# Optimization experiments

Measured on AMD Instinct MI355X. Metric: run time of the kernel, lower is better.

Reference implementation:

```python
import jax, jax.numpy as jnp
import numpy as np

N, FIN, H, C, D = 50000, 128, 4, 64, 4
E = 800000


def leaky_relu(x, slope):
    return jnp.where(x >= 0, x, slope * x)


def gat_layer(x, src, dst, W, A, att_src, att_dst, bias):
    # x: [N, Fin]; W: [Fin, H*C]; A: [Fin, H*D]; att_*: [H, D]; bias: [C]
    n = x.shape[0]
    h = (x @ W).reshape(n, H, -1)          # [N, H, C] message features
    a = (x @ A).reshape(n, H, -1)          # [N, H, D] attention features
    alpha_src = jnp.einsum('nhd,hd->nh', a, att_src)   # [N, H]
    alpha_dst = jnp.einsum('nhd,hd->nh', a, att_dst)   # [N, H]
    e = leaky_relu(alpha_src[src] + alpha_dst[dst], 0.2)  # [E, H]
    # edge softmax over incoming edges of each destination node
    m = jax.ops.segment_max(e, dst, num_segments=n)       # [N, H]
    ex = jnp.exp(e - m[dst])                               # [E, H]
    denom = jax.ops.segment_sum(ex, dst, num_segments=n)  # [N, H]
    w = ex / denom[dst]                                    # [E, H]
    msg = h[src] * w[..., None]                            # [E, H, C]
    out = jax.ops.segment_sum(msg, dst, num_segments=n)   # [N, H, C]
    return out.mean(axis=1) + bias                         # head-average -> [N, C]


def setup_inputs() -> dict:
    key = jax.random.key(0)
    ks = jax.random.split(key, 12)
    x = jax.random.normal(ks[0], (N, FIN), dtype=jnp.float32)
    edge_index = jax.random.randint(ks[1], (2, E), 0, N, dtype=jnp.int64)
    s = 0.05
    return {
        'x': x,
        'edge_index': edge_index,
        'W1': jax.random.normal(ks[2], (FIN, H * C), dtype=jnp.float32) * s,
        'A1': jax.random.normal(ks[3], (FIN, H * D), dtype=jnp.float32) * s,
        'att_src1': jax.random.normal(ks[4], (H, D), dtype=jnp.float32) * s,
        'att_dst1': jax.random.normal(ks[5], (H, D), dtype=jnp.float32) * s,
        'b1': jnp.zeros((C,), dtype=jnp.float32),
        'W2': jax.random.normal(ks[6], (C, H * C), dtype=jnp.float32) * s,
        'A2': jax.random.normal(ks[7], (C, H * D), dtype=jnp.float32) * s,
        'att_src2': jax.random.normal(ks[8], (H, D), dtype=jnp.float32) * s,
        'att_dst2': jax.random.normal(ks[9], (H, D), dtype=jnp.float32) * s,
        'b2': jnp.zeros((C,), dtype=jnp.float32),
    }


def reference(x, edge_index, W1, A1, att_src1, att_dst1, b1, W2, A2, att_src2, att_dst2, b2):
    src, dst = edge_index[0], edge_index[1]
    x = gat_layer(x, src, dst, W1, A1, att_src1, att_dst1, b1)
    x = leaky_relu(x, 0.1)
    x = gat_layer(x, src, dst, W2, A2, att_src2, att_dst2, b2)
    x = leaky_relu(x, 0.1)
    return x
```

## Files before the change

### kernel.cpp

```cpp
#include <hip/hip_runtime.h>


#define N_NODES 50000
#define N_EDGES 800000
#define CAP 64
#define NB_SC4 782
#define NB_NODE1 782
#define NB_SETUP 197

typedef __attribute__((ext_vector_type(8))) short short8;
typedef __attribute__((ext_vector_type(8))) _Float16 f16x8;
typedef __attribute__((ext_vector_type(4))) float f32x4;
typedef __attribute__((ext_vector_type(8))) unsigned short ushort8;
typedef __attribute__((ext_vector_type(4))) unsigned short us4v;

__device__ __forceinline__ float bf2f(unsigned short u){
  return __uint_as_float(((unsigned int)u) << 16);
}
__device__ __forceinline__ unsigned short f2bf(float f){
  unsigned int u = __float_as_uint(f);
  u = (u + 0x7FFFu + ((u >> 16) & 1u)) >> 16;
  return (unsigned short)u;
}
__device__ __forceinline__ float ldf(const void* p, int i, bool bf){
  return bf ? bf2f(((const unsigned short*)p)[i]) : ((const float*)p)[i];
}

struct SetupPtrs {
  const void *W1, *A1, *aS1, *aD1, *b1, *W2, *A2, *aS2, *aD2, *b2, *x;
};


__device__ __forceinline__ void nodeA1_body(int nblk, int tid,
    const void* __restrict__ xin_, const void* __restrict__ A1,
    const void* __restrict__ aS1, const void* __restrict__ aD1,
    float* __restrict__ alpha_s, float* __restrict__ alpha_d)
{
  const int F = 128, STR = F + 8, KT = 4, CH = F / 8;
  __shared__ unsigned short xs[64 * 136];
  __shared__ unsigned short BsdL[2048];
  __shared__ int sbf;
  const int base = nblk * 64;
  if (tid < 64){
    unsigned int wv = ((const unsigned int*)xin_)[tid] & 0xFFFFu;
    unsigned int ex = (wv >> 7) & 0xFFu;
    bool hit = (ex >= 100u && ex <= 135u);
    unsigned long long mm = __ballot(hit);
    if (tid == 0) sbf = (__popcll(mm) > 40) ? 1 : 0;
  }
  __syncthreads();
  const bool bf = (sbf != 0);

  {
    const int lane = tid & 63, kt = tid >> 6, c = lane & 15;
    ushort8 v8;
    #pragma unroll
    for (int j = 0; j < 8; ++j){
      int k = kt * 32 + (lane >> 4) * 8 + j;
      float v = 0.f;
      if (c < 4){
        #pragma unroll
        for (int dd = 0; dd < 4; ++dd)
          v += ldf(A1, k * 16 + c * 4 + dd, bf) * ldf(aS1, c * 4 + dd, bf);
      } else if (c < 8){
        int hh = c - 4;
        #pragma unroll
        for (int dd = 0; dd < 4; ++dd)
          v += ldf(A1, k * 16 + hh * 4 + dd, bf) * ldf(aD1, hh * 4 + dd, bf);
      }
      v8[j] = f2bf(v);
    }
    *(ushort8*)&BsdL[tid * 8] = v8;
  }

  for (int v = tid; v < 64 * CH; v += 256){
    int row = v / CH, c8 = v % CH;
    int node = base + row; if (node >= N_NODES) node = N_NODES - 1;
    size_t g = (size_t)node * F + c8 * 8;
    ushort8 u;
    if (bf){
      u = *(const ushort8*)((const unsigned short*)xin_ + g);
    } else {
      const float* xf = (const float*)xin_ + g;
      float4 f0 = *(const float4*)xf, f1 = *(const float4*)(xf + 4);
      u[0]=f2bf(f0.x); u[1]=f2bf(f0.y); u[2]=f2bf(f0.z); u[3]=f2bf(f0.w);
      u[4]=f2bf(f1.x); u[5]=f2bf(f1.y); u[6]=f2bf(f1.z); u[7]=f2bf(f1.w);
    }
    *(ushort8*)&xs[row * STR + c8 * 8] = u;
  }
  __syncthreads();

  const int wave = tid >> 6, l = tid & 63;
  const int quad = l >> 4, m = l & 15;
  const int wbase = base + wave * 16;

  f32x4 aacc = (f32x4)0.f;
  #pragma unroll
  for (int kt = 0; kt < KT; ++kt){
    short8 af = *(const short8*)&xs[(wave * 16 + m) * STR + kt * 32 + quad * 8];
    short8 sd = *(const short8*)&BsdL[((size_t)kt * 64 + l) * 8];
    aacc = __builtin_amdgcn_mfma_f32_16x16x32_bf16(af, sd, aacc, 0, 0, 0);
  }
  if (m < 8){
    float* dstp = (m < 4) ? alpha_s : alpha_d;
    int hh = m & 3;
    #pragma unroll
    for (int r = 0; r < 4; ++r){
      int node = wbase + quad * 4 + r;
      if (node < N_NODES) dstp[node * 4 + hh] = aacc[r];
    }
  }
}


__global__ __launch_bounds__(256) void k_mega(SetupPtrs S,
    const int* __restrict__ src, const int* __restrict__ dst,
    int* __restrict__ fill, unsigned short* __restrict__ csr,
    float* __restrict__ alpha_s, float* __restrict__ alpha_d,
    _Float16* __restrict__ Wb1f, _Float16* __restrict__ Wb2f,
    unsigned short* __restrict__ Bsd2f,
    float* __restrict__ bc1, float* __restrict__ bc2,
    int* __restrict__ flag)
{
  const int b = blockIdx.x, tid = threadIdx.x;
  if (b < NB_SC4){
    const int ebase = b * 1024 + tid;
    int d[4], s[4];
    #pragma unroll
    for (int i = 0; i < 4; ++i){
      int e = ebase + i * 256;
      bool ok = (e < N_EDGES);
      d[i] = ok ? dst[e] : -1;
      s[i] = ok ? src[e] : 0;
    }
    #pragma unroll
    for (int i = 0; i < 4; ++i){
      if (d[i] >= 0){
        int r = atomicAdd(&fill[d[i]], 1);
        if (r < CAP) csr[((unsigned)d[i] << 6) + r] = (unsigned short)s[i];
      }
    }
    return;
  }
  if (b < NB_SC4 + NB_NODE1){
    nodeA1_body(b - NB_SC4, tid, S.x, S.A1, S.aS1, S.aD1, alpha_s, alpha_d);
    return;
  }
  __shared__ int sbf;
  if (tid < 64){
    unsigned int w = ((const unsigned int*)S.x)[tid] & 0xFFFFu;
    unsigned int e = (w >> 7) & 0xFFu;
    bool hit = (e >= 100u && e <= 135u);
    unsigned long long m = __ballot(hit);
    if (tid == 0) sbf = (__popcll(m) > 40) ? 1 : 0;
  }
  __syncthreads();
  const bool bf = (sbf != 0);
  const int bw = b - NB_SC4 - NB_NODE1;
  if (bw < 128){
    int t = bw * 256 + tid;
    int j = t & 7, lane = (t >> 3) & 63, kt = (t >> 9) & 15, nt = t >> 13;
    int q = kt * 32 + (lane >> 4) * 8 + j;
    int c = nt * 16 + (lane & 15);
    int h = q >> 7, f = q & 127;
    Wb1f[t] = (_Float16)(0.25f * ldf(S.W1, f * 256 + h * 64 + c, bf));
  } else if (bw < 192){
    int t = (bw - 128) * 256 + tid;
    int j = t & 7, lane = (t >> 3) & 63, kt = (t >> 9) & 7, nt = t >> 12;
    int q = kt * 32 + (lane >> 4) * 8 + j;
    int c = nt * 16 + (lane & 15);
    int h = q >> 6, f = q & 63;
    Wb2f[t] = (_Float16)(0.25f * ldf(S.W2, f * 256 + h * 64 + c, bf));
  } else if (bw < 196){
    int t = (bw - 192) * 256 + tid;
    int j = t & 7, lane = (t >> 3) & 63, kt = t >> 9;
    int k = kt * 32 + (lane >> 4) * 8 + j;
    int c = lane & 15;
    float v = 0.f;
    if (c < 4){
      for (int dd = 0; dd < 4; ++dd)
        v += ldf(S.A2, k * 16 + c * 4 + dd, bf) * ldf(S.aS2, c * 4 + dd, bf);
    } else if (c < 8){
      int h = c - 4;
      for (int dd = 0; dd < 4; ++dd)
        v += ldf(S.A2, k * 16 + h * 4 + dd, bf) * ldf(S.aD2, h * 4 + dd, bf);
    }
    Bsd2f[t] = f2bf(v);
  } else {
    if (tid < 64)       bc1[tid] = ldf(S.b1, tid, bf);
    else if (tid < 128) bc2[tid - 64] = ldf(S.b2, tid - 64, bf);
    else if (tid == 128) *flag = bf ? 1 : 0;
  }
}


template<int FIN, bool BF>
__device__ __forceinline__ void ldrow(const void* xg, unsigned s, int f0,
                                      float (&out)[FIN / 16])
{
  const int NFL = FIN / 16;
  if (BF){
    const unsigned short* p = (const unsigned short*)xg + (size_t)s * FIN + f0;
    if (NFL == 8){
      ushort8 u = *(const ushort8*)p;
      #pragma unroll
      for (int j = 0; j < NFL; ++j) out[j] = bf2f(u[j]);
    } else {
      us4v u = *(const us4v*)p;
      #pragma unroll
      for (int j = 0; j < NFL; ++j) out[j] = bf2f(u[j]);
    }
  } else {
    const float* p = (const float*)xg + (size_t)s * FIN + f0;
    #pragma unroll
    for (int j = 0; j < NFL; ++j) out[j] = p[j];
  }
}

template<int FIN, bool BF, int STR>
__device__ __forceinline__ void aggr_phase1(const void* __restrict__ xg,
    const float* __restrict__ alpha_s, const float* __restrict__ alpha_d,
    const int* __restrict__ fill, const unsigned short* __restrict__ csr,
    _Float16* __restrict__ ylds, int base, int w, int l)
{
  const int NFL = FIN / 16;
  const int h = l >> 4, sub = l & 15, f0 = sub * NFL;
  #pragma unroll 1
  for (int r = 0; r < 4; ++r){
    const int n = base + w * 4 + r;
    const float adv = alpha_d[n * 4 + h];
    float den = 0.f;
    float acc[NFL];
    #pragma unroll
    for (int j = 0; j < NFL; ++j) acc[j] = 0.f;

    int cnt = fill[n]; if (cnt > CAP) cnt = CAP;
    const unsigned short* cp = csr + ((unsigned)n << 6);
    int p = 0;
    for (; p + 8 <= cnt; p += 8){
      ushort8 s8 = *(const ushort8*)(cp + p);
      float a[8];
      float v[8][NFL];
      #pragma unroll
      for (int i = 0; i < 8; ++i){
        unsigned s = s8[i];
        a[i] = alpha_s[s * 4 + h];
        ldrow<FIN, BF>(xg, s, f0, v[i]);
      }
      #pragma unroll
      for (int i = 0; i < 8; ++i){
        float e = a[i] + adv; e = fmaxf(e, 0.2f * e); float wt = __expf(e);
        den += wt;
        #pragma unroll
        for (int j = 0; j < NFL; ++j) acc[j] += wt * v[i][j];
      }
    }
    if (p + 4 <= cnt){
      ushort4 s4 = *(const ushort4*)(cp + p);
      unsigned sx = s4.x, sy = s4.y, sz = s4.z, sw = s4.w;
      float ax = alpha_s[sx * 4 + h];
      float ay = alpha_s[sy * 4 + h];
      float az = alpha_s[sz * 4 + h];
      float aw = alpha_s[sw * 4 + h];
      float vx[NFL], vy[NFL], vz[NFL], vw[NFL];
      ldrow<FIN, BF>(xg, sx, f0, vx);
      ldrow<FIN, BF>(xg, sy, f0, vy);
      ldrow<FIN, BF>(xg, sz, f0, vz);
      ldrow<FIN, BF>(xg, sw, f0, vw);
      float e0 = ax + adv; e0 = fmaxf(e0, 0.2f * e0); float w0 = __expf(e0);
      float e1 = ay + adv; e1 = fmaxf(e1, 0.2f * e1); float w1 = __expf(e1);
      float e2 = az + adv; e2 = fmaxf(e2, 0.2f * e2); float w2 = __expf(e2);
      float e3 = aw + adv; e3 = fmaxf(e3, 0.2f * e3); float w3 = __expf(e3);
      den += w0; den += w1; den += w2; den += w3;
      #pragma unroll
      for (int j = 0; j < NFL; ++j)
        acc[j] += w0 * vx[j] + w1 * vy[j] + w2 * vz[j] + w3 * vw[j];
      p += 4;
    }
    for (; p < cnt; ++p){
      unsigned s = cp[p];
      float a = alpha_s[s * 4 + h];
      float v0[NFL];
      ldrow<FIN, BF>(xg, s, f0, v0);
      float e = a + adv; e = fmaxf(e, 0.2f * e); float wgt = __expf(e);
      den += wgt;
      #pragma unroll
      for (int j = 0; j < NFL; ++j) acc[j] += wgt * v0[j];
    }
    const float rh = (den > 0.f) ? (1.f / den) : 0.f;
    const int row = w * 4 + r;
    _Float16* yp = &ylds[row * STR + h * FIN + f0];
    #pragma unroll
    for (int j = 0; j < NFL; ++j) yp[j] = (_Float16)(acc[j] * rh);
  }
}

template<int FIN, int MODE>
__global__ __launch_bounds__(256) void k_aggrX(
    const void* __restrict__ xg,
    const float* __restrict__ alpha_s, const float* __restrict__ alpha_d,
    const int* __restrict__ fill, const unsigned short* __restrict__ csr,
    const _Float16* __restrict__ Wf,
    const float* __restrict__ bias, void* __restrict__ out,
    const int* __restrict__ flag,
    const unsigned short* __restrict__ Bsd2f,
    float* __restrict__ as2, float* __restrict__ ad2)
{
  const int K = 4 * FIN, KT = K / 32, STR = K + 8;
  __shared__ _Float16 ylds[16 * (4 * FIN + 8)];
  __shared__ unsigned short x2t[16 * 72];
  const int tid = threadIdx.x, w = tid >> 6, l = tid & 63;
  const int base = blockIdx.x * 16;

  if (MODE == 0 && *flag == 0)
    aggr_phase1<FIN, false, STR>(xg, alpha_s, alpha_d, fill, csr, ylds, base, w, l);
  else
    aggr_phase1<FIN, true,  STR>(xg, alpha_s, alpha_d, fill, csr, ylds, base, w, l);
  __syncthreads();

  const int quad = l >> 4, m = l & 15;
  const int nt = w;
  f32x4 cacc = (f32x4)0.f;
  #pragma unroll
  for (int kt = 0; kt < KT; ++kt){
    f16x8 av = *(const f16x8*)&ylds[m * STR + kt * 32 + quad * 8];
    f16x8 bv = *(const f16x8*)(Wf + ((size_t)(nt * KT + kt) * 64 + l) * 8);
    cacc = __builtin_amdgcn_mfma_f32_16x16x32_f16(av, bv, cacc, 0, 0, 0);
  }
  const int c = nt * 16 + m;
  const float bs = bias[c];
  #pragma unroll
  for (int r2 = 0; r2 < 4; ++r2){
    int node = base + quad * 4 + r2;
    float v = cacc[r2] + bs;
    v = fmaxf(v, 0.1f * v);
    if (MODE == 0){
      unsigned short o = f2bf(v);
      ((unsigned short*)out)[(size_t)node * 64 + c] = o;
      x2t[(quad * 4 + r2) * 72 + c] = o;
    } else {
      if (*flag) ((unsigned short*)out)[(size_t)node * 64 + c] = f2bf(v);
      else       ((float*)out)[(size_t)node * 64 + c] = v;
    }
  }

  if (MODE == 0){
    __syncthreads();
    if (w == 0){
      f32x4 aacc = (f32x4)0.f;
      #pragma unroll
      for (int kt = 0; kt < 2; ++kt){
        short8 af = *(const short8*)&x2t[m * 72 + kt * 32 + quad * 8];
        short8 sd = *(const short8*)(Bsd2f + ((size_t)kt * 64 + l) * 8);
        aacc = __builtin_amdgcn_mfma_f32_16x16x32_bf16(af, sd, aacc, 0, 0, 0);
      }
      if (m < 8){
        float* dstp = (m < 4) ? as2 : ad2;
        int hh = m & 3;
        #pragma unroll
        for (int r = 0; r < 4; ++r){
          int node = base + quad * 4 + r;
          dstp[node * 4 + hh] = aacc[r];
        }
      }
    }
  }
}


extern "C" void kernel_launch(void* const* d_in, const int* in_sizes, int n_in,
                              void* d_out, int out_size, void* d_ws, size_t ws_size,
                              hipStream_t stream)
{
  const void* x  = d_in[0];
  const int* ei  = (const int*)d_in[1];
  const int* src = ei;
  const int* dst = ei + N_EDGES;

  char* ws = (char*)d_ws;
  unsigned short* csr = (unsigned short*)(ws);
  unsigned short* x2  = (unsigned short*)(ws + 6400000);
  float* as_    = (float*)(ws + 12800000);
  float* ad_    = (float*)(ws + 13600000);
  float* as2_   = (float*)(ws + 14400000);
  float* ad2_   = (float*)(ws + 15200000);
  int*   fill   = (int*)  (ws + 16000000);
  _Float16* Wb1f = (_Float16*)(ws + 16200000);
  _Float16* Wb2f = (_Float16*)(ws + 16265536);
  unsigned short* Bsd2f = (unsigned short*)(ws + 16298304);
  float* bc1    = (float*)(ws + 16300352);
  float* bc2    = (float*)(ws + 16300608);
  int*   flag   = (int*)  (ws + 16300864);

  hipMemsetAsync(fill, 0, N_NODES * sizeof(int), stream);

  SetupPtrs S;
  S.W1 = d_in[2];  S.A1 = d_in[3];  S.aS1 = d_in[4];  S.aD1 = d_in[5];  S.b1 = d_in[6];
  S.W2 = d_in[7];  S.A2 = d_in[8];  S.aS2 = d_in[9];  S.aD2 = d_in[10]; S.b2 = d_in[11];
  S.x  = x;

  k_mega<<<NB_SC4 + NB_NODE1 + NB_SETUP, 256, 0, stream>>>(
      S, src, dst, fill, csr, as_, ad_, Wb1f, Wb2f, Bsd2f, bc1, bc2, flag);

  k_aggrX<128, 0><<<N_NODES / 16, 256, 0, stream>>>(
      x, as_, ad_, fill, csr, Wb1f, bc1, x2, flag, Bsd2f, as2_, ad2_);

  k_aggrX<64, 1><<<N_NODES / 16, 256, 0, stream>>>(
      x2, as2_, ad2_, fill, csr, Wb2f, bc2, d_out, flag, Bsd2f, as2_, ad2_);
}
```

Before: 298.9 us.

## Bucket incoming edges by source-index slice and gather in sorted slice order

The CSR build now splits each destination's edge list into 8 buckets keyed by the high bits of the source index. The aggregation kernel compacts these buckets into shared memory, then walks the slices in order across all four rows of a wave, so gathers of source rows land in a narrower address range at a time, which should improve cache locality. The costs are an 8x larger fill counter array with a bigger memset, extra shared-memory staging with two barriers, and a 16-edge cap per slice that could drop edges for nodes whose incoming edges cluster in one slice.

```diff
diff --git a/kernel.cpp b/kernel.cpp
--- a/kernel.cpp
+++ b/kernel.cpp
@@ -3,7 +3,9 @@
 
 #define N_NODES 50000
 #define N_EDGES 800000
-#define CAP 64
+#define SLICES 8
+#define SCAP 16
+#define NCAP 64
 #define NB_SC4 782
 #define NB_NODE1 782
 #define NB_SETUP 197
@@ -136,8 +138,10 @@
     #pragma unroll
     for (int i = 0; i < 4; ++i){
       if (d[i] >= 0){
-        int r = atomicAdd(&fill[d[i]], 1);
-        if (r < CAP) csr[((unsigned)d[i] << 6) + r] = (unsigned short)s[i];
+        unsigned sl = ((unsigned)s[i]) >> 13;
+        unsigned bidx = (unsigned)d[i] * SLICES + sl;
+        int r = atomicAdd(&fill[bidx], 1);
+        if (r < SCAP) csr[(bidx << 4) + r] = (unsigned short)s[i];
       }
     }
     return;
@@ -220,78 +224,67 @@
 template<int FIN, bool BF, int STR>
 __device__ __forceinline__ void aggr_phase1(const void* __restrict__ xg,
     const float* __restrict__ alpha_s, const float* __restrict__ alpha_d,
-    const int* __restrict__ fill, const unsigned short* __restrict__ csr,
+    const unsigned short (*__restrict__ els)[NCAP], const int (*__restrict__ sst)[SLICES + 1],
     _Float16* __restrict__ ylds, int base, int w, int l)
 {
   const int NFL = FIN / 16;
   const int h = l >> 4, sub = l & 15, f0 = sub * NFL;
-  #pragma unroll 1
+  const int j0 = w * 4;
+
+  float den[4] = {0.f, 0.f, 0.f, 0.f};
+  float acc[4][NFL];
+  #pragma unroll
+  for (int r = 0; r < 4; ++r)
+    #pragma unroll
+    for (int j = 0; j < NFL; ++j) acc[r][j] = 0.f;
+  float adv[4];
+  #pragma unroll
+  for (int r = 0; r < 4; ++r) adv[r] = alpha_d[(base + j0 + r) * 4 + h];
+
+  for (int sl = 0; sl < SLICES; ++sl){
+    #pragma unroll
+    for (int r = 0; r < 4; ++r){
+      const unsigned short* cp = els[j0 + r];
+      int p  = sst[j0 + r][sl];
+      int en = sst[j0 + r][sl + 1];
+      for (; p + 4 <= en; p += 4){
+        unsigned sx = cp[p], sy = cp[p+1], sz = cp[p+2], sw = cp[p+3];
+        float ax = alpha_s[sx * 4 + h];
+        float ay = alpha_s[sy * 4 + h];
+        float az = alpha_s[sz * 4 + h];
+        float aw = alpha_s[sw * 4 + h];
+        float vx[NFL], vy[NFL], vz[NFL], vw[NFL];
+        ldrow<FIN, BF>(xg, sx, f0, vx);
+        ldrow<FIN, BF>(xg, sy, f0, vy);
+        ldrow<FIN, BF>(xg, sz, f0, vz);
+        ldrow<FIN, BF>(xg, sw, f0, vw);
+        float e0 = ax + adv[r]; e0 = fmaxf(e0, 0.2f * e0); float w0 = __expf(e0);
+        float e1 = ay + adv[r]; e1 = fmaxf(e1, 0.2f * e1); float w1 = __expf(e1);
+        float e2 = az + adv[r]; e2 = fmaxf(e2, 0.2f * e2); float w2 = __expf(e2);
+        float e3 = aw + adv[r]; e3 = fmaxf(e3, 0.2f * e3); float w3 = __expf(e3);
+        den[r] += w0; den[r] += w1; den[r] += w2; den[r] += w3;
+        #pragma unroll
+        for (int j = 0; j < NFL; ++j)
+          acc[r][j] += w0 * vx[j] + w1 * vy[j] + w2 * vz[j] + w3 * vw[j];
+      }
+      for (; p < en; ++p){
+        unsigned s = cp[p];
+        float a = alpha_s[s * 4 + h];
+        float v0[NFL];
+        ldrow<FIN, BF>(xg, s, f0, v0);
+        float e = a + adv[r]; e = fmaxf(e, 0.2f * e); float wgt = __expf(e);
+        den[r] += wgt;
+        #pragma unroll
+        for (int j = 0; j < NFL; ++j) acc[r][j] += wgt * v0[j];
+      }
+    }
+  }
+  #pragma unroll
   for (int r = 0; r < 4; ++r){
-    const int n = base + w * 4 + r;
-    const float adv = alpha_d[n * 4 + h];
-    float den = 0.f;
-    float acc[NFL];
-    #pragma unroll
-    for (int j = 0; j < NFL; ++j) acc[j] = 0.f;
-
-    int cnt = fill[n]; if (cnt > CAP) cnt = CAP;
-    const unsigned short* cp = csr + ((unsigned)n << 6);
-    int p = 0;
-    for (; p + 8 <= cnt; p += 8){
-      ushort8 s8 = *(const ushort8*)(cp + p);
-      float a[8];
-      float v[8][NFL];
-      #pragma unroll
-      for (int i = 0; i < 8; ++i){
-        unsigned s = s8[i];
-        a[i] = alpha_s[s * 4 + h];
-        ldrow<FIN, BF>(xg, s, f0, v[i]);
-      }
-      #pragma unroll
-      for (int i = 0; i < 8; ++i){
-        float e = a[i] + adv; e = fmaxf(e, 0.2f * e); float wt = __expf(e);
-        den += wt;
-        #pragma unroll
-        for (int j = 0; j < NFL; ++j) acc[j] += wt * v[i][j];
-      }
-    }
-    if (p + 4 <= cnt){
-      ushort4 s4 = *(const ushort4*)(cp + p);
-      unsigned sx = s4.x, sy = s4.y, sz = s4.z, sw = s4.w;
-      float ax = alpha_s[sx * 4 + h];
-      float ay = alpha_s[sy * 4 + h];
-      float az = alpha_s[sz * 4 + h];
-      float aw = alpha_s[sw * 4 + h];
-      float vx[NFL], vy[NFL], vz[NFL], vw[NFL];
-      ldrow<FIN, BF>(xg, sx, f0, vx);
-      ldrow<FIN, BF>(xg, sy, f0, vy);
-      ldrow<FIN, BF>(xg, sz, f0, vz);
-      ldrow<FIN, BF>(xg, sw, f0, vw);
-      float e0 = ax + adv; e0 = fmaxf(e0, 0.2f * e0); float w0 = __expf(e0);
-      float e1 = ay + adv; e1 = fmaxf(e1, 0.2f * e1); float w1 = __expf(e1);
-      float e2 = az + adv; e2 = fmaxf(e2, 0.2f * e2); float w2 = __expf(e2);
-      float e3 = aw + adv; e3 = fmaxf(e3, 0.2f * e3); float w3 = __expf(e3);
-      den += w0; den += w1; den += w2; den += w3;
-      #pragma unroll
-      for (int j = 0; j < NFL; ++j)
-        acc[j] += w0 * vx[j] + w1 * vy[j] + w2 * vz[j] + w3 * vw[j];
-      p += 4;
-    }
-    for (; p < cnt; ++p){
-      unsigned s = cp[p];
-      float a = alpha_s[s * 4 + h];
-      float v0[NFL];
-      ldrow<FIN, BF>(xg, s, f0, v0);
-      float e = a + adv; e = fmaxf(e, 0.2f * e); float wgt = __expf(e);
-      den += wgt;
-      #pragma unroll
-      for (int j = 0; j < NFL; ++j) acc[j] += wgt * v0[j];
-    }
-    const float rh = (den > 0.f) ? (1.f / den) : 0.f;
-    const int row = w * 4 + r;
-    _Float16* yp = &ylds[row * STR + h * FIN + f0];
-    #pragma unroll
-    for (int j = 0; j < NFL; ++j) yp[j] = (_Float16)(acc[j] * rh);
+    const float rh = (den[r] > 0.f) ? (1.f / den[r]) : 0.f;
+    _Float16* yp = &ylds[(j0 + r) * STR + h * FIN + f0];
+    #pragma unroll
+    for (int j = 0; j < NFL; ++j) yp[j] = (_Float16)(acc[r][j] * rh);
   }
 }
 
@@ -309,13 +302,48 @@
   const int K = 4 * FIN, KT = K / 32, STR = K + 8;
   __shared__ _Float16 ylds[16 * (4 * FIN + 8)];
   __shared__ unsigned short x2t[16 * 72];
+  __shared__ unsigned short els[16][NCAP];
+  __shared__ int sst[16][SLICES + 1];
+  __shared__ int cs_[16][SLICES];
   const int tid = threadIdx.x, w = tid >> 6, l = tid & 63;
   const int base = blockIdx.x * 16;
 
+  if (tid < 128){
+    int j = tid >> 3, sl = tid & 7;
+    int c = fill[(base + j) * SLICES + sl];
+    cs_[j][sl] = (c > SCAP) ? SCAP : c;
+  }
+  __syncthreads();
+  if (tid < 16){
+    int s0 = 0;
+    sst[tid][0] = 0;
+    #pragma unroll
+    for (int sl = 0; sl < SLICES; ++sl){
+      int c = cs_[tid][sl];
+      if (s0 + c > NCAP) c = NCAP - s0;
+      s0 += c;
+      sst[tid][sl + 1] = s0;
+    }
+  }
+  __syncthreads();
+  if (tid < 128){
+    int j = tid >> 3, sl = tid & 7;
+    int st = sst[j][sl], c = sst[j][sl + 1] - st;
+    const unsigned short* gp = csr + ((((unsigned)(base + j)) * SLICES + sl) << 4);
+    ushort8 v0 = *(const ushort8*)gp;
+    ushort8 v1 = *(const ushort8*)(gp + 8);
+    #pragma unroll
+    for (int q = 0; q < 16; ++q){
+      unsigned short vq = (q < 8) ? v0[q] : v1[q - 8];
+      if (q < c) els[j][st + q] = vq;
+    }
+  }
+  __syncthreads();
+
   if (MODE == 0 && *flag == 0)
-    aggr_phase1<FIN, false, STR>(xg, alpha_s, alpha_d, fill, csr, ylds, base, w, l);
+    aggr_phase1<FIN, false, STR>(xg, alpha_s, alpha_d, els, sst, ylds, base, w, l);
   else
-    aggr_phase1<FIN, true,  STR>(xg, alpha_s, alpha_d, fill, csr, ylds, base, w, l);
+    aggr_phase1<FIN, true,  STR>(xg, alpha_s, alpha_d, els, sst, ylds, base, w, l);
   __syncthreads();
 
   const int quad = l >> 4, m = l & 15;
@@ -379,20 +407,20 @@
 
   char* ws = (char*)d_ws;
   unsigned short* csr = (unsigned short*)(ws);
-  unsigned short* x2  = (unsigned short*)(ws + 6400000);
-  float* as_    = (float*)(ws + 12800000);
-  float* ad_    = (float*)(ws + 13600000);
-  float* as2_   = (float*)(ws + 14400000);
-  float* ad2_   = (float*)(ws + 15200000);
-  int*   fill   = (int*)  (ws + 16000000);
-  _Float16* Wb1f = (_Float16*)(ws + 16200000);
-  _Float16* Wb2f = (_Float16*)(ws + 16265536);
-  unsigned short* Bsd2f = (unsigned short*)(ws + 16298304);
-  float* bc1    = (float*)(ws + 16300352);
-  float* bc2    = (float*)(ws + 16300608);
-  int*   flag   = (int*)  (ws + 16300864);
-
-  hipMemsetAsync(fill, 0, N_NODES * sizeof(int), stream);
+  unsigned short* x2  = (unsigned short*)(ws + 12800000);
+  float* as_    = (float*)(ws + 19200000);
+  float* ad_    = (float*)(ws + 20000000);
+  float* as2_   = (float*)(ws + 20800000);
+  float* ad2_   = (float*)(ws + 21600000);
+  int*   fill   = (int*)  (ws + 22400000);
+  _Float16* Wb1f = (_Float16*)(ws + 24000000);
+  _Float16* Wb2f = (_Float16*)(ws + 24065536);
+  unsigned short* Bsd2f = (unsigned short*)(ws + 24098304);
+  float* bc1    = (float*)(ws + 24100352);
+  float* bc2    = (float*)(ws + 24100608);
+  int*   flag   = (int*)  (ws + 24100864);
+
+  hipMemsetAsync(fill, 0, N_NODES * SLICES * sizeof(int), stream);
 
   SetupPtrs S;
   S.W1 = d_in[2];  S.A1 = d_in[3];  S.aS1 = d_in[4];  S.aD1 = d_in[5];  S.b1 = d_in[6];
```

New measurement: 338.6 us. +13.3%, slower.
